# Optimization experiments

Hardware: AMD Instinct MI355X
Metric: run time of the kernel (lower is better)

The kernel has to match this reference:

```python
import jax, jax.numpy as jnp
import numpy as np

V, E, H, F, A, L = 32000, 256, 512, 512, 256, 49  # vocab, embed, hidden, feature, attn, n_locations
B, T = 64, 32


def setup_inputs() -> dict:
    key = jax.random.key(0)
    ks = jax.random.split(key, 16)
    s = lambda k, sh: (jax.random.normal(k, sh, jnp.float32) * 0.02)
    embedding = s(ks[0], (V, E)).at[0].set(0.0)  # padding_idx=0 row zeroed
    return dict(
        image_feats=jax.random.normal(ks[1], (B, L, F), jnp.float32),
        caption_in=jax.random.randint(ks[2], (B, T), 0, V, dtype=jnp.int32),
        embedding=embedding,
        W_init_h=s(ks[3], (F, H)), b_init_h=jnp.zeros((H,), jnp.float32),
        W_init_c=s(ks[4], (F, H)), b_init_c=jnp.zeros((H,), jnp.float32),
        W_feat=s(ks[5], (F, A)), b_feat=jnp.zeros((A,), jnp.float32),
        W_hid=s(ks[6], (H, A)), b_hid=jnp.zeros((A,), jnp.float32),
        W_score=s(ks[7], (A,)), b_score=jnp.zeros((), jnp.float32),
        W_ih=s(ks[8], (E + F, 4 * H)), b_ih=jnp.zeros((4 * H,), jnp.float32),
        W_hh=s(ks[9], (H, 4 * H)), b_hh=jnp.zeros((4 * H,), jnp.float32),
        W_out=s(ks[10], (H, V)), b_out=jnp.zeros((V,), jnp.float32),
    )


def reference(image_feats, caption_in, embedding,
              W_init_h, b_init_h, W_init_c, b_init_c,
              W_feat, b_feat, W_hid, b_hid, W_score, b_score,
              W_ih, b_ih, W_hh, b_hh, W_out, b_out):
    # init_hidden_state: mean over spatial locations -> two linears
    mean_feats = image_feats.mean(axis=1)                      # (B, F)
    h0 = mean_feats @ W_init_h + b_init_h                      # (B, H)
    c0 = mean_feats @ W_init_c + b_init_c                      # (B, H)
    embs = embedding[caption_in]                               # (B, T, E); dropout = identity (eval)
    feat_proj = image_feats @ W_feat + b_feat                  # (B, L, A) - invariant over t, precompute

    def step(carry, emb_t):
        h, c = carry
        # additive attention
        energy = jnp.tanh(feat_proj + (h @ W_hid + b_hid)[:, None, :])   # (B, L, A)
        scores = energy @ W_score + b_score                              # (B, L)
        alpha = jax.nn.softmax(scores, axis=1)                           # (B, L)
        context = jnp.einsum('bl,blf->bf', alpha, image_feats)           # (B, F)
        # LSTMCell (torch gate order i, f, g, o)
        x = jnp.concatenate([emb_t, context], axis=1)                    # (B, E+F)
        gates = x @ W_ih + b_ih + h @ W_hh + b_hh                        # (B, 4H)
        i, f, g, o = jnp.split(gates, 4, axis=1)
        i = jax.nn.sigmoid(i); f = jax.nn.sigmoid(f); o = jax.nn.sigmoid(o)
        c_new = f * c + i * jnp.tanh(g)
        h_new = o * jnp.tanh(c_new)
        logits_t = h_new @ W_out + b_out                                 # (B, V); dropout = identity
        return (h_new, c_new), (logits_t, alpha)

    _, (logits, alphas) = jax.lax.scan(step, (h0, c0), jnp.swapaxes(embs, 0, 1))
    predictions = jnp.swapaxes(logits, 0, 1)   # (B, T, V)
    all_alphas = jnp.swapaxes(alphas, 0, 1)    # (B, T, L)
    return predictions, all_alphas
```

## Files before the change

kernel.cpp:

```cpp
#include <hip/hip_runtime.h>
#include <hip/hip_bf16.h>

typedef _Float16 f16;
typedef _Float16 f16x8 __attribute__((ext_vector_type(8)));
typedef _Float16 f16x4 __attribute__((ext_vector_type(4)));
typedef _Float16 f16x2 __attribute__((ext_vector_type(2)));
typedef float f32x4 __attribute__((ext_vector_type(4)));
typedef unsigned long long ull;

#define B_ 64
#define T_ 32
#define L_ 49
#define F_ 512
#define H_ 512
#define A_ 256
#define E_ 256
#define V_ 32000
#define G4 2048
#define NG 64
#define NLOG 125
#define SLOT 16

#define ALOAD32(p)     __hip_atomic_load((const unsigned*)(p), __ATOMIC_RELAXED, __HIP_MEMORY_SCOPE_AGENT)
#define ASTORE32(p, v) __hip_atomic_store((unsigned*)(p), (v), __ATOMIC_RELAXED, __HIP_MEMORY_SCOPE_AGENT)
#define ASTORE64(p, v) __hip_atomic_store((ull*)(p), (v), __ATOMIC_RELAXED, __HIP_MEMORY_SCOPE_AGENT)

#if defined(__has_builtin)
#if __has_builtin(__builtin_amdgcn_fdot2)
#define HAS_FDOT2 1
#endif
#endif

#define NB_TC0 (64 * 24)
#define NB_TC1 (64 * 16)
#define NB_TC2 (1000 * 16)
#define NB_PAIR 256
#define NB_CVT 1568
#define NB_EMB 2048
#define NB_INIT 64
#define NB_FP  196

__device__ void dev_tcvt(const float* __restrict__ x, f16* __restrict__ y,
                         int R, int C, int bx, int by, char* smem) {
    float (*ls)[33] = (float(*)[33])smem;
    int c0 = bx * 32, r0 = by * 32;
    int tid = threadIdx.x;
    int rr = tid >> 3, cs = (tid & 7) * 4;
    float4 v = *(const float4*)&x[(size_t)(r0 + rr) * C + c0 + cs];
    ls[rr][cs] = v.x; ls[rr][cs + 1] = v.y; ls[rr][cs + 2] = v.z; ls[rr][cs + 3] = v.w;
    __syncthreads();
    int cr = tid >> 3, rs = (tid & 7) * 4;
    f16x4 o = {(f16)ls[rs][cr], (f16)ls[rs + 1][cr], (f16)ls[rs + 2][cr], (f16)ls[rs + 3][cr]};
    *(f16x4*)&y[(size_t)(c0 + cr) * R + r0 + rs] = o;
}

__global__ __launch_bounds__(256) void k_prep(
    const float* __restrict__ image_feats, const int* __restrict__ caption,
    const float* __restrict__ embedding,
    const float* __restrict__ W_init_h, const float* __restrict__ b_init_h,
    const float* __restrict__ W_init_c, const float* __restrict__ b_init_c,
    const float* __restrict__ W_feat, const float* __restrict__ b_feat,
    const float* __restrict__ W_hid, const float* __restrict__ W_ih,
    const float* __restrict__ W_hh, const float* __restrict__ W_out,
    f16* __restrict__ feats16, f16* __restrict__ embs16,
    f16* __restrict__ WihT, f16* __restrict__ WhhT,
    f16* __restrict__ WoutT, f16* __restrict__ Whidp,
    f16* __restrict__ hslab, float* __restrict__ c_cur,
    float* __restrict__ featproj) {
    __shared__ __align__(16) char smem[32768];
    int bid = blockIdx.x, tid = threadIdx.x;
    int r = bid;
    if (r < NB_TC0) { dev_tcvt(W_ih, WihT, E_ + F_, G4, r % 64, r / 64, smem); return; }
    r -= NB_TC0;
    if (r < NB_TC1) { dev_tcvt(W_hh, WhhT, H_, G4, r % 64, r / 64, smem); return; }
    r -= NB_TC1;
    if (r < NB_TC2) { dev_tcvt(W_out, WoutT, H_, V_, r % 1000, r / 1000, smem); return; }
    r -= NB_TC2;
    if (r < NB_PAIR) {
        int k2 = r;
        Whidp[(k2 * 256 + tid) * 2]     = (f16)W_hid[(2 * k2) * 256 + tid];
        Whidp[(k2 * 256 + tid) * 2 + 1] = (f16)W_hid[(2 * k2 + 1) * 256 + tid];
        return;
    }
    r -= NB_PAIR;
    if (r < NB_CVT) {
        int i = r * 256 + tid;
        float4 v = ((const float4*)image_feats)[i];
        f16x4 h = {(f16)v.x, (f16)v.y, (f16)v.z, (f16)v.w};
        ((f16x4*)feats16)[i] = h;
        return;
    }
    r -= NB_CVT;
    if (r < NB_EMB) {
        int tok = caption[r];
        embs16[(size_t)r * E_ + tid] = (f16)embedding[(size_t)tok * E_ + tid];
        return;
    }
    r -= NB_EMB;
    if (r < NB_INIT) {
        float* mean = (float*)smem;
        int b = r;
        for (int f = tid; f < F_; f += 256) {
            float s = 0.f;
            for (int l = 0; l < L_; ++l) s += image_feats[((size_t)b * L_ + l) * F_ + f];
            mean[f] = s * (1.f / 49.f);
        }
        __syncthreads();
        for (int h = tid; h < H_; h += 256) {
            float a = b_init_h[h], c = b_init_c[h];
            for (int k = 0; k < F_; ++k) {
                float m = mean[k];
                a += m * W_init_h[k * H_ + h];
                c += m * W_init_c[k * H_ + h];
            }
            hslab[(size_t)b * H_ + h] = (f16)a;
            c_cur[b * H_ + h] = c;
        }
        return;
    }
    r -= NB_INIT;
    {
        float (*fs)[F_] = (float(*)[F_])smem;
        int r0 = r * 16;
        for (int i = tid; i < 16 * F_; i += 256)
            fs[i >> 9][i & 511] = image_feats[(size_t)r0 * F_ + i];
        __syncthreads();
        float acc[16];
#pragma unroll
        for (int q = 0; q < 16; ++q) acc[q] = 0.f;
        for (int k = 0; k < F_; ++k) {
            float w = W_feat[k * A_ + tid];
#pragma unroll
            for (int q = 0; q < 16; ++q) acc[q] += fs[q][k] * w;
        }
        float bb = b_feat[tid];
#pragma unroll
        for (int q = 0; q < 16; ++q) featproj[(size_t)(r0 + q) * A_ + tid] = acc[q] + bb;
    }
}

struct Smem128 { f16 As[128][40]; f16 Bs[128][40]; };

__global__ __launch_bounds__(256) void k_gemm_emb(
    const f16* __restrict__ A, const f16* __restrict__ Bt,
    f16* __restrict__ Cv, const float* __restrict__ bias0, const float* __restrict__ bias1) {
    __shared__ Smem128 sm;
    int bid = blockIdx.x;
    int mtiles = B_ * T_ / 128;
    int m0 = (bid % mtiles) * 128, n0 = (bid / mtiles) * 128;
    int tid = threadIdx.x, lane = tid & 63, wave = tid >> 6;
    int wr = (wave >> 1) * 64, wc = (wave & 1) * 64;
    int frow = lane & 15, fk = (lane >> 4) * 8;
    int ra = tid >> 2, ka = (tid & 3) * 8;
    f32x4 acc[4][4];
#pragma unroll
    for (int i = 0; i < 4; ++i)
#pragma unroll
        for (int j = 0; j < 4; ++j) { acc[i][j][0]=0.f; acc[i][j][1]=0.f; acc[i][j][2]=0.f; acc[i][j][3]=0.f; }
    for (int k0 = 0; k0 < E_; k0 += 32) {
        f16x8 a0 = *(const f16x8*)&A[(size_t)(m0 + ra) * E_ + k0 + ka];
        f16x8 a1 = *(const f16x8*)&A[(size_t)(m0 + 64 + ra) * E_ + k0 + ka];
        f16x8 b0 = *(const f16x8*)&Bt[(size_t)(n0 + ra) * (E_ + F_) + k0 + ka];
        f16x8 b1 = *(const f16x8*)&Bt[(size_t)(n0 + 64 + ra) * (E_ + F_) + k0 + ka];
        __syncthreads();
        *(f16x8*)&sm.As[ra][ka] = a0;
        *(f16x8*)&sm.As[64 + ra][ka] = a1;
        *(f16x8*)&sm.Bs[ra][ka] = b0;
        *(f16x8*)&sm.Bs[64 + ra][ka] = b1;
        __syncthreads();
        f16x8 av[4], bv[4];
#pragma unroll
        for (int i = 0; i < 4; ++i) {
            av[i] = *(f16x8*)&sm.As[wr + i * 16 + frow][fk];
            bv[i] = *(f16x8*)&sm.Bs[wc + i * 16 + frow][fk];
        }
#pragma unroll
        for (int mi = 0; mi < 4; ++mi)
#pragma unroll
            for (int ni = 0; ni < 4; ++ni)
                acc[mi][ni] = __builtin_amdgcn_mfma_f32_16x16x32_f16(av[mi], bv[ni], acc[mi][ni], 0, 0, 0);
    }
    int rq = (lane >> 4) * 4;
#pragma unroll
    for (int mi = 0; mi < 4; ++mi)
#pragma unroll
        for (int ni = 0; ni < 4; ++ni) {
            int cc = n0 + wc + ni * 16 + frow;
            float badd = bias0[cc] + bias1[cc];
#pragma unroll
            for (int r = 0; r < 4; ++r) {
                int rr = m0 + wr + mi * 16 + rq + r;
                Cv[((size_t)rr * 512 + (cc & 511)) * 4 + (cc >> 9)] =
                    (f16)(acc[mi][ni][r] + badd);
            }
        }
}

struct GateSm {
    float fp[L_][A_];
    unsigned fe[L_ * 256];
    float ea[A_];
    float ws[A_];
    float sc[64];
    float alpha[64];
    unsigned hL[256];
};
struct GemmSm {
    f16 w[32][512];
    f16 w2[32][512];
    union {
        f16 hs[64][512];
        f16 hwT16[64][40];
    } u;
};
struct LogSm { f16 hs[128][512]; };

__device__ __forceinline__ void wait_n(const unsigned* flags, int n, unsigned target) {
    int tid = threadIdx.x;
    if (tid < n) {
        const unsigned* p = flags + tid * SLOT;
        while (ALOAD32(p) < target) __builtin_amdgcn_s_sleep(1);
    }
    asm volatile("" ::: "memory");
    __syncthreads();
}

__device__ __forceinline__ float sigm(float x) { return 1.f / (1.f + __expf(-x)); }
__device__ __forceinline__ float tanh_f(float x) { return 1.f - 2.f / (1.f + __expf(2.f * x)); }

__global__ __launch_bounds__(256, 1) void k_steps(
    const f16* __restrict__ WhhT, const f16* __restrict__ WihT,
    const f16* __restrict__ Whidp,
    const float* __restrict__ featproj, const f16* __restrict__ feats16,
    const float* __restrict__ b_hid,
    const float* __restrict__ W_score, const float* __restrict__ b_score,
    const f16* __restrict__ embP, const float* __restrict__ c_cur,
    f16* __restrict__ hslab, f16* __restrict__ ctxslab, f16* __restrict__ hwcslab,
    const f16* __restrict__ WoutT, const float* __restrict__ b_out,
    float* __restrict__ preds, float* __restrict__ out_alpha,
    unsigned* __restrict__ gateflag, unsigned* __restrict__ ctxflag,
    unsigned* __restrict__ gemmflag) {
    __shared__ __align__(16) char smraw[sizeof(LogSm)];
    int bid = blockIdx.x, tid = threadIdx.x;

    if (bid < 64) {
        int b = bid;
        GateSm* S = (GateSm*)smraw;
        for (int i = tid; i < L_ * A_; i += 256)
            ((float*)S->fp)[i] = featproj[(size_t)b * L_ * A_ + i];
        {
            const f16x8* src = (const f16x8*)(feats16 + (size_t)b * L_ * F_);
            f16x8* dst = (f16x8*)S->fe;
            for (int i = tid; i < L_ * F_ / 8; i += 256) dst[i] = src[i];
        }
        S->ws[tid] = W_score[tid];
        float bhid_r = b_hid[tid];
        float bsc = b_score[0];
        S->hL[tid] = ((const unsigned*)hslab)[(size_t)b * 256 + tid];
        float cs0 = c_cur[b * H_ + 2 * tid], cs1 = c_cur[b * H_ + 2 * tid + 1];
        const unsigned* wp32 = (const unsigned*)Whidp;
        int wv = tid >> 6, ln = tid & 63;
        __syncthreads();

        for (int t = 0; t < T_; ++t) {
            {
                float acc = bhid_r;
#pragma unroll 16
                for (int k2 = 0; k2 < 256; ++k2) {
                    union { unsigned u; f16x2 v; } w, h;
                    w.u = wp32[k2 * 256 + tid];
                    h.u = S->hL[k2];
#ifdef HAS_FDOT2
                    acc = __builtin_amdgcn_fdot2(w.v, h.v, acc, false);
#else
                    acc += (float)w.v.x * (float)h.v.x + (float)w.v.y * (float)h.v.y;
#endif
                }
                S->ea[tid] = acc;
            }
            __syncthreads();
            for (int l = wv; l < L_; l += 4) {
                float p = 0.f;
#pragma unroll
                for (int q = 0; q < 4; ++q) {
                    int j = ln + q * 64;
                    p += tanh_f(S->fp[l][j] + S->ea[j]) * S->ws[j];
                }
#pragma unroll
                for (int off = 32; off > 0; off >>= 1) p += __shfl_xor(p, off);
                if (ln == 0) S->sc[l] = p;
            }
            __syncthreads();
            if (tid < 64) {
                float v = (tid < L_) ? S->sc[tid] + bsc : -3.4e38f;
                float m = v;
#pragma unroll
                for (int off = 32; off > 0; off >>= 1) m = fmaxf(m, __shfl_xor(m, off));
                float e = (tid < L_) ? __expf(v - m) : 0.f;
                float s = e;
#pragma unroll
                for (int off = 32; off > 0; off >>= 1) s += __shfl_xor(s, off);
                if (tid < L_) {
                    float al = e / s;
                    S->alpha[tid] = al;
                    out_alpha[((size_t)b * T_ + t) * L_ + tid] = al;
                }
            }
            __syncthreads();
            {
                float c0 = 0.f, c1 = 0.f;
#pragma unroll 7
                for (int l = 0; l < L_; ++l) {
                    float a = S->alpha[l];
                    union { unsigned u; f16x2 v; } fv;
                    fv.u = S->fe[l * 256 + tid];
                    c0 += a * (float)fv.v.x;
                    c1 += a * (float)fv.v.y;
                }
                union { f16 h[2]; unsigned u; } pk;
                pk.h[0] = (f16)c0; pk.h[1] = (f16)c1;
                ASTORE32((unsigned*)ctxslab + ((size_t)t * B_ + b) * 256 + tid, pk.u);
            }
            __syncthreads();
            if (tid == 0) ASTORE32(&ctxflag[b * SLOT], (unsigned)(t + 1));
            f16x8 ep = *(const f16x8*)&embP[((size_t)b * T_ + t) * G4 + 8 * tid];
            wait_n(gemmflag, NG, (unsigned)(t + 1));
            {
                f16x8 hw = *(const f16x8*)&hwcslab[((size_t)t * B_ + b) * G4 + 8 * tid];
                float gA[8];
#pragma unroll
                for (int i = 0; i < 8; ++i) gA[i] = (float)hw[i] + (float)ep[i];
                float cn0 = sigm(gA[1]) * cs0 + sigm(gA[0]) * tanh_f(gA[2]);
                float cn1 = sigm(gA[5]) * cs1 + sigm(gA[4]) * tanh_f(gA[6]);
                float hn0 = sigm(gA[3]) * tanh_f(cn0);
                float hn1 = sigm(gA[7]) * tanh_f(cn1);
                cs0 = cn0; cs1 = cn1;
                union { f16 h[2]; unsigned u; } pk;
                pk.h[0] = (f16)hn0; pk.h[1] = (f16)hn1;
                S->hL[tid] = pk.u;
                ASTORE32((unsigned*)hslab + ((size_t)(t + 1) * B_ + b) * 256 + tid, pk.u);
            }
            __syncthreads();
            if (tid == 0)
                ASTORE32(&gateflag[b * SLOT], (unsigned)(t + 2));
        }
    } else if (bid < 64 + NG) {
        int g = bid - 64;
        GemmSm* S = (GemmSm*)smraw;
        for (int i = 0; i < 8; ++i) {
            int idx = i * 256 + tid;
            int r = idx >> 6, ch = idx & 63;
            int cc = (r & 3) * 512 + 8 * g + (r >> 2);
            *(f16x8*)&S->w[r][(ch ^ (r & 7)) * 8] =
                *(const f16x8*)&WhhT[(size_t)cc * 512 + ch * 8];
            *(f16x8*)&S->w2[r][(ch ^ (r & 7)) * 8] =
                *(const f16x8*)&WihT[(size_t)cc * (E_ + F_) + E_ + ch * 8];
        }
        int wvv = tid >> 6, lane = tid & 63;
        int frow = lane & 15, q = lane >> 4, sw = frow & 7, rq = q * 4;
        int mb = (wvv >> 1) * 32, c16 = (wvv & 1) * 16;
        int bo = tid >> 2, cq = (tid & 3) * 8;
        __syncthreads();

        for (int t = 0; t < T_; ++t) {
            if (t) wait_n(gateflag, 64, (unsigned)(t + 1));
            {
                const f16* hsrc = hslab + (size_t)t * B_ * H_;
#pragma unroll
                for (int i = 0; i < 16; ++i) {
                    int idx = i * 256 + tid;
                    int r = idx >> 6, ch = idx & 63;
                    *(f16x8*)&S->u.hs[r][(ch ^ (r & 7)) * 8] =
                        *(const f16x8*)&hsrc[(size_t)r * H_ + ch * 8];
                }
            }
            __syncthreads();
            f32x4 a4[2];
            a4[0][0]=0.f; a4[0][1]=0.f; a4[0][2]=0.f; a4[0][3]=0.f;
            a4[1][0]=0.f; a4[1][1]=0.f; a4[1][2]=0.f; a4[1][3]=0.f;
#pragma unroll
            for (int kk = 0; kk < 16; ++kk) {
                int ch = ((kk * 4 + q) ^ sw) * 8;
                f16x8 bv = *(f16x8*)&S->w[c16 + frow][ch];
                f16x8 av0 = *(f16x8*)&S->u.hs[mb + frow][ch];
                f16x8 av1 = *(f16x8*)&S->u.hs[mb + 16 + frow][ch];
                a4[0] = __builtin_amdgcn_mfma_f32_16x16x32_f16(av0, bv, a4[0], 0, 0, 0);
                a4[1] = __builtin_amdgcn_mfma_f32_16x16x32_f16(av1, bv, a4[1], 0, 0, 0);
            }
            wait_n(ctxflag, 64, (unsigned)(t + 1));
            {
                const f16* csrc = ctxslab + (size_t)t * B_ * F_;
#pragma unroll
                for (int i = 0; i < 16; ++i) {
                    int idx = i * 256 + tid;
                    int r = idx >> 6, ch = idx & 63;
                    *(f16x8*)&S->u.hs[r][(ch ^ (r & 7)) * 8] =
                        *(const f16x8*)&csrc[(size_t)r * F_ + ch * 8];
                }
            }
            __syncthreads();
#pragma unroll
            for (int kk = 0; kk < 16; ++kk) {
                int ch = ((kk * 4 + q) ^ sw) * 8;
                f16x8 bv = *(f16x8*)&S->w2[c16 + frow][ch];
                f16x8 av0 = *(f16x8*)&S->u.hs[mb + frow][ch];
                f16x8 av1 = *(f16x8*)&S->u.hs[mb + 16 + frow][ch];
                a4[0] = __builtin_amdgcn_mfma_f32_16x16x32_f16(av0, bv, a4[0], 0, 0, 0);
                a4[1] = __builtin_amdgcn_mfma_f32_16x16x32_f16(av1, bv, a4[1], 0, 0, 0);
            }
            __syncthreads();
#pragma unroll
            for (int mi = 0; mi < 2; ++mi)
#pragma unroll
                for (int r = 0; r < 4; ++r)
                    S->u.hwT16[mb + mi * 16 + rq + r][c16 + frow] = (f16)a4[mi][r];
            __syncthreads();
            {
                f16* dst = hwcslab + ((size_t)t * B_ + bo) * G4 + 32 * g + cq;
                union { f16 h[4]; ull u; } pk0, pk1;
                *(f16x4*)pk0.h = *(f16x4*)&S->u.hwT16[bo][cq];
                *(f16x4*)pk1.h = *(f16x4*)&S->u.hwT16[bo][cq + 4];
                ASTORE64(dst, pk0.u);
                ASTORE64(dst + 4, pk1.u);
            }
            __syncthreads();
            if (tid == 0)
                ASTORE32(&gemmflag[g * SLOT], (unsigned)(t + 1));
        }
    } else {
        int nt = bid - 64 - NG;
        int n0 = nt * 256;
        LogSm* S = (LogSm*)smraw;
        int wvv = tid >> 6, lane = tid & 63;
        int frow = lane & 15, q = lane >> 4, sw = frow & 7, rq = q * 4;

        for (int tc = 0; tc < T_ / 2; ++tc) {
            wait_n(gateflag, 64, (unsigned)(2 * tc + 3));
            {
                const f16* hsrc = hslab + (size_t)(2 * tc + 1) * B_ * H_;
#pragma unroll
                for (int i = 0; i < 32; ++i) {
                    int idx = i * 256 + tid;
                    int r = idx >> 6, ch = idx & 63;
                    *(f16x8*)&S->hs[r][(ch ^ (r & 7)) * 8] =
                        *(const f16x8*)&hsrc[(size_t)r * H_ + ch * 8];
                }
            }
            __syncthreads();
            f32x4 acc[8][4];
#pragma unroll
            for (int mi = 0; mi < 8; ++mi)
#pragma unroll
                for (int ni = 0; ni < 4; ++ni) { acc[mi][ni][0]=0.f; acc[mi][ni][1]=0.f; acc[mi][ni][2]=0.f; acc[mi][ni][3]=0.f; }
#pragma unroll 2
            for (int kk = 0; kk < 16; ++kk) {
                int ch = ((kk * 4 + q) ^ sw) * 8;
                f16x8 av[8], bv[4];
#pragma unroll
                for (int mi = 0; mi < 8; ++mi)
                    av[mi] = *(f16x8*)&S->hs[mi * 16 + frow][ch];
#pragma unroll
                for (int ni = 0; ni < 4; ++ni)
                    bv[ni] = *(const f16x8*)&WoutT[(size_t)(n0 + wvv * 64 + ni * 16 + frow) * 512 + kk * 32 + q * 8];
#pragma unroll
                for (int mi = 0; mi < 8; ++mi)
#pragma unroll
                    for (int ni = 0; ni < 4; ++ni)
                        acc[mi][ni] = __builtin_amdgcn_mfma_f32_16x16x32_f16(av[mi], bv[ni], acc[mi][ni], 0, 0, 0);
            }
#pragma unroll
            for (int ni = 0; ni < 4; ++ni) {
                int cc = n0 + wvv * 64 + ni * 16 + frow;
                float badd = b_out[cc];
#pragma unroll
                for (int mi = 0; mi < 8; ++mi)
#pragma unroll
                    for (int r = 0; r < 4; ++r) {
                        int rr = mi * 16 + rq + r;
                        int tt = 2 * tc + (rr >> 6), bb2 = rr & 63;
                        preds[((size_t)bb2 * T_ + tt) * V_ + cc] = acc[mi][ni][r] + badd;
                    }
            }
            __syncthreads();
        }
    }
}

extern "C" void kernel_launch(void* const* d_in, const int* in_sizes, int n_in,
                              void* d_out, int out_size, void* d_ws, size_t ws_size,
                              hipStream_t stream) {
    const float* image_feats = (const float*)d_in[0];
    const int*   caption     = (const int*)d_in[1];
    const float* embedding   = (const float*)d_in[2];
    const float* W_init_h    = (const float*)d_in[3];
    const float* b_init_h    = (const float*)d_in[4];
    const float* W_init_c    = (const float*)d_in[5];
    const float* b_init_c    = (const float*)d_in[6];
    const float* W_feat      = (const float*)d_in[7];
    const float* b_feat      = (const float*)d_in[8];
    const float* W_hid       = (const float*)d_in[9];
    const float* b_hid       = (const float*)d_in[10];
    const float* W_score     = (const float*)d_in[11];
    const float* b_score     = (const float*)d_in[12];
    const float* W_ih        = (const float*)d_in[13];
    const float* b_ih        = (const float*)d_in[14];
    const float* W_hh        = (const float*)d_in[15];
    const float* b_hh        = (const float*)d_in[16];
    const float* W_out       = (const float*)d_in[17];
    const float* b_out       = (const float*)d_in[18];

    float* preds = (float*)d_out;
    float* out_alpha = preds + (size_t)B_ * T_ * V_;

    size_t off = 0;
    char* base = (char*)d_ws;
    auto carve = [&](size_t bytes) {
        void* p = base + off;
        off += (bytes + 255) & ~(size_t)255;
        return p;
    };
    f16* embP       = (f16*)carve((size_t)B_ * T_ * G4 * 2);
    float* featproj = (float*)carve((size_t)B_ * L_ * A_ * 4);
    float* c_cur    = (float*)carve((size_t)B_ * H_ * 4);
    f16* hslab      = (f16*)carve((size_t)(T_ + 1) * B_ * H_ * 2);
    f16* ctxslab    = (f16*)carve((size_t)T_ * B_ * F_ * 2);
    f16* hwcslab    = (f16*)carve((size_t)T_ * B_ * G4 * 2);
    unsigned* flags = (unsigned*)carve((64 + 64 + NG) * SLOT * 4);
    f16* feats16    = (f16*)carve((size_t)B_ * L_ * F_ * 2);
    f16* embs16     = (f16*)carve((size_t)B_ * T_ * E_ * 2);
    f16* WihT       = (f16*)carve((size_t)G4 * (E_ + F_) * 2);
    f16* WhhT       = (f16*)carve((size_t)G4 * H_ * 2);
    f16* WoutT      = (f16*)carve((size_t)V_ * H_ * 2);
    f16* Whidp      = (f16*)carve((size_t)H_ * A_ * 2);
    unsigned* gateflag = flags;
    unsigned* ctxflag  = flags + 64 * SLOT;
    unsigned* gemmflag = flags + 128 * SLOT;
    (void)ws_size; (void)in_sizes; (void)n_in; (void)out_size;

    {
        int nb = NB_TC0 + NB_TC1 + NB_TC2 + NB_PAIR + NB_CVT + NB_EMB + NB_INIT + NB_FP;
        hipLaunchKernelGGL(k_prep, dim3(nb), dim3(256), 0, stream,
                           image_feats, caption, embedding,
                           W_init_h, b_init_h, W_init_c, b_init_c,
                           W_feat, b_feat, W_hid, W_ih, W_hh, W_out,
                           feats16, embs16, WihT, WhhT, WoutT, Whidp,
                           hslab, c_cur, featproj);
    }
    hipLaunchKernelGGL(k_gemm_emb, dim3((B_ * T_ / 128) * (G4 / 128)), dim3(256), 0, stream,
                       embs16, WihT, embP, b_ih, b_hh);
    hipMemsetAsync(flags, 0, (64 + 64 + NG) * SLOT * 4, stream);
    hipLaunchKernelGGL(k_steps, dim3(64 + NG + NLOG), dim3(256), 0, stream,
                       WhhT, WihT, Whidp, featproj, feats16, b_hid,
                       W_score, b_score, embP, c_cur,
                       hslab, ctxslab, hwcslab,
                       WoutT, b_out, preds, out_alpha,
                       gateflag, ctxflag, gemmflag);
}
```

Baseline: 668.9 us.

## Move W_out transpose into idle logits blocks and widen W_hid loads

The 16000-block W_out fp32-to-fp16 transpose moves out of the prep kernel and into the logits blocks of the persistent step kernel. Those blocks would otherwise sit idle waiting for the first hidden states, so the conversion is meant to overlap with the recurrent gate work. W_hid is repacked into groups of four so the attention projection loop issues one 8-byte load per two fdot2 ops. The logits blocks' spin-wait also sleeps longer between polls to reduce contention on the flags. The risk is that the transpose delays the first logits tile, and the longer sleep adds wake-up latency.

```diff
diff --git a/kernel.cpp b/kernel.cpp
--- a/kernel.cpp
+++ b/kernel.cpp
@@ -33,8 +33,7 @@
 
 #define NB_TC0 (64 * 24)
 #define NB_TC1 (64 * 16)
-#define NB_TC2 (1000 * 16)
-#define NB_PAIR 256
+#define NB_Q   128
 #define NB_CVT 1568
 #define NB_EMB 2048
 #define NB_INIT 64
@@ -61,10 +60,10 @@
     const float* __restrict__ W_init_c, const float* __restrict__ b_init_c,
     const float* __restrict__ W_feat, const float* __restrict__ b_feat,
     const float* __restrict__ W_hid, const float* __restrict__ W_ih,
-    const float* __restrict__ W_hh, const float* __restrict__ W_out,
+    const float* __restrict__ W_hh,
     f16* __restrict__ feats16, f16* __restrict__ embs16,
     f16* __restrict__ WihT, f16* __restrict__ WhhT,
-    f16* __restrict__ WoutT, f16* __restrict__ Whidp,
+    f16* __restrict__ Whidp,
     f16* __restrict__ hslab, float* __restrict__ c_cur,
     float* __restrict__ featproj) {
     __shared__ __align__(16) char smem[32768];
@@ -74,15 +73,15 @@
     r -= NB_TC0;
     if (r < NB_TC1) { dev_tcvt(W_hh, WhhT, H_, G4, r % 64, r / 64, smem); return; }
     r -= NB_TC1;
-    if (r < NB_TC2) { dev_tcvt(W_out, WoutT, H_, V_, r % 1000, r / 1000, smem); return; }
-    r -= NB_TC2;
-    if (r < NB_PAIR) {
-        int k2 = r;
-        Whidp[(k2 * 256 + tid) * 2]     = (f16)W_hid[(2 * k2) * 256 + tid];
-        Whidp[(k2 * 256 + tid) * 2 + 1] = (f16)W_hid[(2 * k2 + 1) * 256 + tid];
+    if (r < NB_Q) {
+        int k4 = r;
+        f16 buf[4];
+#pragma unroll
+        for (int j = 0; j < 4; ++j) buf[j] = (f16)W_hid[(size_t)(4 * k4 + j) * 256 + tid];
+        *(f16x4*)&Whidp[((size_t)k4 * 256 + tid) * 4] = *(f16x4*)buf;
         return;
     }
-    r -= NB_PAIR;
+    r -= NB_Q;
     if (r < NB_CVT) {
         int i = r * 256 + tid;
         float4 v = ((const float4*)image_feats)[i];
@@ -225,6 +224,16 @@
     __syncthreads();
 }
 
+__device__ __forceinline__ void wait_n_slow(const unsigned* flags, int n, unsigned target) {
+    int tid = threadIdx.x;
+    if (tid < n) {
+        const unsigned* p = flags + tid * SLOT;
+        while (ALOAD32(p) < target) __builtin_amdgcn_s_sleep(8);
+    }
+    asm volatile("" ::: "memory");
+    __syncthreads();
+}
+
 __device__ __forceinline__ float sigm(float x) { return 1.f / (1.f + __expf(-x)); }
 __device__ __forceinline__ float tanh_f(float x) { return 1.f - 2.f / (1.f + __expf(2.f * x)); }
 
@@ -236,7 +245,8 @@
     const float* __restrict__ W_score, const float* __restrict__ b_score,
     const f16* __restrict__ embP, const float* __restrict__ c_cur,
     f16* __restrict__ hslab, f16* __restrict__ ctxslab, f16* __restrict__ hwcslab,
-    const f16* __restrict__ WoutT, const float* __restrict__ b_out,
+    const float* __restrict__ W_out, f16* __restrict__ WoutT,
+    const float* __restrict__ b_out,
     float* __restrict__ preds, float* __restrict__ out_alpha,
     unsigned* __restrict__ gateflag, unsigned* __restrict__ ctxflag,
     unsigned* __restrict__ gemmflag) {
@@ -258,7 +268,7 @@
         float bsc = b_score[0];
         S->hL[tid] = ((const unsigned*)hslab)[(size_t)b * 256 + tid];
         float cs0 = c_cur[b * H_ + 2 * tid], cs1 = c_cur[b * H_ + 2 * tid + 1];
-        const unsigned* wp32 = (const unsigned*)Whidp;
+        const f16x4* wp4 = (const f16x4*)Whidp;
         int wv = tid >> 6, ln = tid & 63;
         __syncthreads();
 
@@ -266,14 +276,18 @@
             {
                 float acc = bhid_r;
 #pragma unroll 16
-                for (int k2 = 0; k2 < 256; ++k2) {
-                    union { unsigned u; f16x2 v; } w, h;
-                    w.u = wp32[k2 * 256 + tid];
-                    h.u = S->hL[k2];
+                for (int k4 = 0; k4 < 128; ++k4) {
+                    union { f16x4 v; f16x2 p[2]; } w;
+                    w.v = wp4[(size_t)k4 * 256 + tid];
+                    union { unsigned u; f16x2 v; } h0, h1;
+                    h0.u = S->hL[2 * k4];
+                    h1.u = S->hL[2 * k4 + 1];
 #ifdef HAS_FDOT2
-                    acc = __builtin_amdgcn_fdot2(w.v, h.v, acc, false);
+                    acc = __builtin_amdgcn_fdot2(w.p[0], h0.v, acc, false);
+                    acc = __builtin_amdgcn_fdot2(w.p[1], h1.v, acc, false);
 #else
-                    acc += (float)w.v.x * (float)h.v.x + (float)w.v.y * (float)h.v.y;
+                    acc += (float)w.p[0].x * (float)h0.v.x + (float)w.p[0].y * (float)h0.v.y;
+                    acc += (float)w.p[1].x * (float)h1.v.x + (float)w.p[1].y * (float)h1.v.y;
 #endif
                 }
                 S->ea[tid] = acc;
@@ -434,8 +448,25 @@
         int wvv = tid >> 6, lane = tid & 63;
         int frow = lane & 15, q = lane >> 4, sw = frow & 7, rq = q * 4;
 
+        {
+            float (*ls)[33] = (float(*)[33])smraw;
+            int rr = tid >> 3, cs = (tid & 7) * 4;
+            int cr = tid >> 3, rs = (tid & 7) * 4;
+            for (int c0 = 0; c0 < 256; c0 += 32)
+                for (int k0 = 0; k0 < 512; k0 += 32) {
+                    float4 v = *(const float4*)&W_out[(size_t)(k0 + rr) * V_ + n0 + c0 + cs];
+                    __syncthreads();
+                    ls[rr][cs] = v.x; ls[rr][cs + 1] = v.y; ls[rr][cs + 2] = v.z; ls[rr][cs + 3] = v.w;
+                    __syncthreads();
+                    f16x4 o = {(f16)ls[rs][cr], (f16)ls[rs + 1][cr],
+                               (f16)ls[rs + 2][cr], (f16)ls[rs + 3][cr]};
+                    *(f16x4*)&WoutT[(size_t)(n0 + c0 + cr) * 512 + k0 + rs] = o;
+                }
+            __syncthreads();
+        }
+
         for (int tc = 0; tc < T_ / 2; ++tc) {
-            wait_n(gateflag, 64, (unsigned)(2 * tc + 3));
+            wait_n_slow(gateflag, 64, (unsigned)(2 * tc + 3));
             {
                 const f16* hsrc = hslab + (size_t)(2 * tc + 1) * B_ * H_;
 #pragma unroll
@@ -538,12 +569,12 @@
     (void)ws_size; (void)in_sizes; (void)n_in; (void)out_size;
 
     {
-        int nb = NB_TC0 + NB_TC1 + NB_TC2 + NB_PAIR + NB_CVT + NB_EMB + NB_INIT + NB_FP;
+        int nb = NB_TC0 + NB_TC1 + NB_Q + NB_CVT + NB_EMB + NB_INIT + NB_FP;
         hipLaunchKernelGGL(k_prep, dim3(nb), dim3(256), 0, stream,
                            image_feats, caption, embedding,
                            W_init_h, b_init_h, W_init_c, b_init_c,
-                           W_feat, b_feat, W_hid, W_ih, W_hh, W_out,
-                           feats16, embs16, WihT, WhhT, WoutT, Whidp,
+                           W_feat, b_feat, W_hid, W_ih, W_hh,
+                           feats16, embs16, WihT, WhhT, Whidp,
                            hslab, c_cur, featproj);
     }
     hipLaunchKernelGGL(k_gemm_emb, dim3((B_ * T_ / 128) * (G4 / 128)), dim3(256), 0, stream,
@@ -553,6 +584,6 @@
                        WhhT, WihT, Whidp, featproj, feats16, b_hid,
                        W_score, b_score, embP, c_cur,
                        hslab, ctxslab, hwcslab,
-                       WoutT, b_out, preds, out_alpha,
+                       W_out, WoutT, b_out, preds, out_alpha,
                        gateflag, ctxflag, gemmflag);
 }
```

Result: faster. 626.4 us (-6.4%).
